# Performance work log

Hardware: AMD Instinct MI355X
Metric: run time of the kernel (lower is better)

The kernel has to match this reference:

```python
import jax, jax.numpy as jnp
import numpy as np

LEAKY_ALPHA = 0.2  # tf.nn.leaky_relu default

def setup_inputs() -> dict:
    key = jax.random.key(0)
    k1, k2, k3 = jax.random.split(key, 3)
    B, N, F, U = 4, 4096, 128, 64
    x = jax.random.normal(k1, (B, N, F), dtype=jnp.float32)
    W = jax.random.normal(k2, (F, U), dtype=jnp.float32) * (1.0 / np.sqrt(F))
    a = jax.random.normal(k3, (2 * U, 1), dtype=jnp.float32) * (1.0 / np.sqrt(2 * U))
    return {"x": x, "W": W, "a": a}

def reference(x, W, a):
    # h: (B, N, U)
    h = jnp.einsum('bnf,fu->bnu', x, W)
    U = h.shape[-1]
    a1 = a[:U, 0]   # attends to source node i
    a2 = a[U:, 0]   # attends to target node j
    # a^T [h_i || h_j] = a1^T h_i + a2^T h_j  (same math, no O(N^2*2U) concat)
    f1 = jnp.einsum('bnu,u->bn', h, a1)  # (B, N)
    f2 = jnp.einsum('bnu,u->bn', h, a2)  # (B, N)
    e = f1[:, :, None] + f2[:, None, :]  # (B, N, N)
    e = jnp.where(e >= 0, e, LEAKY_ALPHA * e)
    attn = jax.nn.softmax(e, axis=-1)    # softmax over j
    return jnp.einsum('bij,bju->biu', attn, h)
```

## Files before the change

kernel.cpp:

```cpp
#include <hip/hip_runtime.h>
#include <hip/hip_bf16.h>

#define NBATCH 4
#define NN 4096
#define NF 128
#define NU 64
#define CH 16
#define NCH (NN / CH)
#define LEAKY 0.2f

__global__ __launch_bounds__(256) void k1_h(
    const float* __restrict__ x, const float* __restrict__ W,
    const float* __restrict__ a,
    float* __restrict__ h, float* __restrict__ f1, float* __restrict__ f2) {
  __shared__ float xs[16][NF];
  int tid = threadIdx.x;
  int row0 = blockIdx.x * 16;
  const float4* xg = (const float4*)(x + (size_t)row0 * NF);
  float4* xs4 = (float4*)xs;
  for (int k = tid; k < 16 * NF / 4; k += 256) xs4[k] = xg[k];
  __syncthreads();
  int u = tid & 63;
  int wv = tid >> 6;
  float acc[4] = {0.f, 0.f, 0.f, 0.f};
#pragma unroll 4
  for (int f = 0; f < NF; f += 4) {
    float w0 = W[(f+0)*NU+u], w1 = W[(f+1)*NU+u],
          w2 = W[(f+2)*NU+u], w3 = W[(f+3)*NU+u];
#pragma unroll
    for (int r = 0; r < 4; ++r) {
      float4 xv = *(const float4*)&xs[wv*4+r][f];
      acc[r] += xv.x*w0 + xv.y*w1 + xv.z*w2 + xv.w*w3;
    }
  }
  float a1 = a[u], a2 = a[NU+u];
#pragma unroll
  for (int r = 0; r < 4; ++r) {
    int grow = row0 + wv*4 + r;
    h[(size_t)grow*NU+u] = acc[r];
    float p1 = acc[r]*a1, p2 = acc[r]*a2;
#pragma unroll
    for (int off = 32; off >= 1; off >>= 1) {
      p1 += __shfl_xor(p1, off, 64);
      p2 += __shfl_xor(p2, off, 64);
    }
    if (u == 0) { f1[grow] = p1; f2[grow] = p2; }
  }
}

__global__ __launch_bounds__(256) void k2a_count(
    const float* __restrict__ f2, unsigned short* __restrict__ pc) {
  __shared__ float fsk[256];
  int b = blockIdx.x >> 7;
  int jc = (blockIdx.x >> 4) & 7;
  int kc = blockIdx.x & 15;
  int tid = threadIdx.x;
  const float* f2b = f2 + b * NN;
  fsk[tid] = f2b[kc * 256 + tid];
  __syncthreads();
  int j0 = jc * 512 + tid;
  int j1 = j0 + 256;
  float my0 = f2b[j0], my1 = f2b[j1];
  int k0g = kc * 256;
  int cnt0 = 0, cnt1 = 0;
#pragma unroll 8
  for (int k = 0; k < 256; k += 4) {
    float4 v = *(const float4*)&fsk[k];
    int kg = k0g + k;
    cnt0 += (v.x < my0) || (v.x == my0 && kg + 0 < j0);
    cnt0 += (v.y < my0) || (v.y == my0 && kg + 1 < j0);
    cnt0 += (v.z < my0) || (v.z == my0 && kg + 2 < j0);
    cnt0 += (v.w < my0) || (v.w == my0 && kg + 3 < j0);
    cnt1 += (v.x < my1) || (v.x == my1 && kg + 0 < j1);
    cnt1 += (v.y < my1) || (v.y == my1 && kg + 1 < j1);
    cnt1 += (v.z < my1) || (v.z == my1 && kg + 2 < j1);
    cnt1 += (v.w < my1) || (v.w == my1 && kg + 3 < j1);
  }
  size_t base = ((size_t)(b * 16 + kc)) * NN;
  pc[base + j0] = (unsigned short)cnt0;
  pc[base + j1] = (unsigned short)cnt1;
}

__global__ __launch_bounds__(256) void k2b_scatter(
    const float* __restrict__ f2, const unsigned short* __restrict__ pc,
    float4* __restrict__ sdat, float* __restrict__ f2s) {
  int b = blockIdx.x >> 4;
  int jc = blockIdx.x & 15;
  int j = jc * 256 + threadIdx.x;
  float my = f2[b * NN + j];
  int rank = 0;
#pragma unroll
  for (int kc = 0; kc < 16; ++kc)
    rank += pc[((size_t)(b * 16 + kc)) * NN + j];
  int o = b * NN + rank;
  float4 v;
  v.x = my; v.y = expf(my); v.z = expf(LEAKY * my); v.w = __int_as_float(j);
  sdat[o] = v;
  f2s[o] = my;
}

__global__ __launch_bounds__(256) void k3_csum(
    const float* __restrict__ h, const float4* __restrict__ sdat,
    float* __restrict__ Pvhi, float* __restrict__ Pvlo,
    float* __restrict__ Pshi, float* __restrict__ Pslo) {
  int u = threadIdx.x & 63;
  int wv = threadIdx.x >> 6;
  int cg = blockIdx.x * 4 + wv;
  int b = cg >> 8;
  int c = cg & (NCH - 1);
  int k0 = b * NN + c * CH;
  const float* hb = h + (size_t)b * NN * NU;
  float ah = 0.f, al = 0.f, sh = 0.f, sl = 0.f;
#pragma unroll
  for (int k = 0; k < CH; ++k) {
    float4 e = sdat[k0 + k];
    int j = __float_as_int(e.w);
    float hv = hb[(size_t)j * NU + u];
    ah += e.y * hv; al += e.z * hv; sh += e.y; sl += e.z;
  }
  size_t o = (size_t)(b * (NCH + 1) + c) * NU + u;
  Pvhi[o] = ah; Pvlo[o] = al;
  if (u == 0) { Pshi[b * (NCH + 1) + c] = sh; Pslo[b * (NCH + 1) + c] = sl; }
}

__global__ __launch_bounds__(256) void k3b_scan(
    float* __restrict__ Pvhi, float* __restrict__ Pvlo,
    float* __restrict__ Pshi, float* __restrict__ Pslo) {
  int wid = blockIdx.x * 4 + (threadIdx.x >> 6);
  int l = threadIdx.x & 63;
  if (wid < 512) {
    int b = wid >> 7;
    int half = (wid >> 6) & 1;
    int u = wid & 63;
    float* T = half ? Pvlo : Pvhi;
    size_t i0 = (size_t)(b * (NCH + 1) + 4 * l) * NU + u;
    float v0 = T[i0], v1 = T[i0 + NU], v2 = T[i0 + 2*NU], v3 = T[i0 + 3*NU];
    float lsum = v0 + v1 + v2 + v3, s = lsum;
#pragma unroll
    for (int off = 1; off < 64; off <<= 1) {
      float t = __shfl_up(s, off, 64);
      if (l >= off) s += t;
    }
    float e = s - lsum;
    T[i0] = e;
    T[i0 + NU] = e + v0;
    T[i0 + 2*NU] = e + v0 + v1;
    T[i0 + 3*NU] = e + v0 + v1 + v2;
    if (l == 63) T[(size_t)(b * (NCH + 1) + NCH) * NU + u] = s;
  } else if (wid < 520) {
    int s2 = wid - 512;
    int b = s2 >> 1;
    float* T = (s2 & 1) ? Pslo : Pshi;
    int i0 = b * (NCH + 1) + 4 * l;
    float v0 = T[i0], v1 = T[i0 + 1], v2 = T[i0 + 2], v3 = T[i0 + 3];
    float lsum = v0 + v1 + v2 + v3, s = lsum;
#pragma unroll
    for (int off = 1; off < 64; off <<= 1) {
      float t = __shfl_up(s, off, 64);
      if (l >= off) s += t;
    }
    float e = s - lsum;
    T[i0] = e; T[i0 + 1] = e + v0; T[i0 + 2] = e + v0 + v1;
    T[i0 + 3] = e + v0 + v1 + v2;
    if (l == 63) T[b * (NCH + 1) + NCH] = s;
  }
}

__global__ __launch_bounds__(256) void k4_out(
    const float* __restrict__ f1, const float* __restrict__ f2s,
    const float* __restrict__ h, const float4* __restrict__ sdat,
    const float* __restrict__ Pvhi, const float* __restrict__ Pvlo,
    const float* __restrict__ Pshi, const float* __restrict__ Pslo,
    float* __restrict__ out) {
  int u = threadIdx.x & 63;
  int wv = threadIdx.x >> 6;
  int row = blockIdx.x * 4 + wv;
  int b = row >> 12;
  const float* fs = f2s + b * NN;
  float fv = f1[row];
  float theta = -fv;
  float q1 = fs[u * 64 + 63];
  int n1 = __popcll(__ballot(q1 < theta));
  int t;
  if (n1 == 64) {
    t = NN;
  } else {
    float q2 = fs[n1 * 64 + u];
    t = n1 * 64 + __popcll(__ballot(q2 < theta));
  }
  int c = t >> 4; if (c > NCH - 1) c = NCH - 1;
  int k0 = b * NN + c * CH;
  const float* hb = h + (size_t)b * NN * NU;
  float ch = 0.f, cl = 0.f, csh = 0.f, csl = 0.f;
#pragma unroll
  for (int k = 0; k < CH; ++k) {
    int kg = c * CH + k;
    float4 e = sdat[k0 + k];
    int j = __float_as_int(e.w);
    float hv = hb[(size_t)j * NU + u];
    bool hi = (kg >= t);
    float wH = hi ? e.y : 0.f;
    float wL = hi ? 0.f : e.z;
    ch += wH * hv; cl += wL * hv; csh += wH; csl += wL;
  }
  size_t base = (size_t)b * (NCH + 1);
  size_t oc0 = (base + c) * NU + u;
  size_t oc1 = (base + c + 1) * NU + u;
  size_t oT  = (base + NCH) * NU + u;
  float Ahi = (Pvhi[oT] - Pvhi[oc1]) + ch;
  float Alo = Pvlo[oc0] + cl;
  float Shi = (Pshi[base + NCH] - Pshi[base + c + 1]) + csh;
  float Slo = Pslo[base + c] + csl;
  float e1 = expf(fv), e1l = expf(LEAKY * fv);
  float den = e1 * Shi + e1l * Slo;
  out[(size_t)row * NU + u] = (e1 * Ahi + e1l * Alo) / den;
}

extern "C" void kernel_launch(void* const* d_in, const int* in_sizes, int n_in,
                              void* d_out, int out_size, void* d_ws, size_t ws_size,
                              hipStream_t stream) {
  const float* x = (const float*)d_in[0];
  const float* W = (const float*)d_in[1];
  const float* a = (const float*)d_in[2];
  float* out = (float*)d_out;
  float* ws = (float*)d_ws;

  size_t o = 0;
  float* h    = ws + o; o += (size_t)NBATCH * NN * NU;
  float* f1   = ws + o; o += (size_t)NBATCH * NN;
  float* f2   = ws + o; o += (size_t)NBATCH * NN;
  float* f2s  = ws + o; o += (size_t)NBATCH * NN;
  float4* sdat = (float4*)(ws + o); o += (size_t)NBATCH * NN * 4;
  float* Pvhi = ws + o; o += (size_t)NBATCH * (NCH + 1) * NU;
  float* Pvlo = ws + o; o += (size_t)NBATCH * (NCH + 1) * NU;
  float* Pshi = ws + o; o += (size_t)NBATCH * (NCH + 1);
  float* Pslo = ws + o; o += (size_t)NBATCH * (NCH + 1);
  unsigned short* pc = (unsigned short*)(ws + o); o += (size_t)NBATCH * 16 * NN / 2;

  k1_h<<<(NBATCH * NN) / 16, 256, 0, stream>>>(x, W, a, h, f1, f2);
  k2a_count<<<512, 256, 0, stream>>>(f2, pc);
  k2b_scatter<<<NBATCH * 16, 256, 0, stream>>>(f2, pc, sdat, f2s);
  k3_csum<<<(NBATCH * NCH) / 4, 256, 0, stream>>>(h, sdat, Pvhi, Pvlo, Pshi, Pslo);
  k3b_scan<<<130, 256, 0, stream>>>(Pvhi, Pvlo, Pshi, Pslo);
  k4_out<<<(NBATCH * NN) / 4, 256, 0, stream>>>(f1, f2s, h, sdat,
      Pvhi, Pvlo, Pshi, Pslo, out);
}
```

Before: 112.5 us.

## Fuse six GAT kernels into one cooperative persistent kernel with grid syncs

Replaces the six separate kernel launches (projection, rank count, scatter, chunk sums, scan, output) with one cooperative kernel of 512 blocks that separates the phases with grid.sync(). Per-block work is resized to fit 512 blocks, for example 32 rows per block in the projection and 8 output rows per wave. The aim is to remove launch and inter-kernel gap overhead, which matters at this small total time. In exchange the kernel depends on cooperative-launch residency and pays for five grid-wide barriers, and some phases leave most threads idle.

Result: slower. 406.4 us (+261.4%).

```diff
diff --git a/kernel.cpp b/kernel.cpp
--- a/kernel.cpp
+++ b/kernel.cpp
@@ -1,5 +1,8 @@
 #include <hip/hip_runtime.h>
+#include <hip/hip_cooperative_groups.h>
 #include <hip/hip_bf16.h>
+
+namespace cg = cooperative_groups;
 
 #define NBATCH 4
 #define NN 4096
@@ -8,212 +11,219 @@
 #define CH 16
 #define NCH (NN / CH)
 #define LEAKY 0.2f
-
-__global__ __launch_bounds__(256) void k1_h(
+#define NB 512
+
+__global__ __launch_bounds__(256, 2) void fused_gat(
     const float* __restrict__ x, const float* __restrict__ W,
-    const float* __restrict__ a,
-    float* __restrict__ h, float* __restrict__ f1, float* __restrict__ f2) {
-  __shared__ float xs[16][NF];
+    const float* __restrict__ a, float* __restrict__ h,
+    float* __restrict__ f1, float* __restrict__ f2,
+    unsigned short* __restrict__ pc, float4* __restrict__ sdat,
+    float* __restrict__ f2s, float* __restrict__ Pvhi,
+    float* __restrict__ Pvlo, float* __restrict__ Pshi,
+    float* __restrict__ Pslo, float* __restrict__ out) {
+  cg::grid_group grid = cg::this_grid();
+  __shared__ float smem[32 * NF];
   int tid = threadIdx.x;
-  int row0 = blockIdx.x * 16;
-  const float4* xg = (const float4*)(x + (size_t)row0 * NF);
-  float4* xs4 = (float4*)xs;
-  for (int k = tid; k < 16 * NF / 4; k += 256) xs4[k] = xg[k];
-  __syncthreads();
-  int u = tid & 63;
+  int blk = blockIdx.x;
+  int lane = tid & 63;
   int wv = tid >> 6;
-  float acc[4] = {0.f, 0.f, 0.f, 0.f};
+
+  {
+    float (*xs)[NF] = (float (*)[NF])smem;
+    int row0 = blk * 32;
+    const float4* xg = (const float4*)(x + (size_t)row0 * NF);
+    float4* xs4 = (float4*)smem;
+    for (int k = tid; k < 32 * NF / 4; k += 256) xs4[k] = xg[k];
+    __syncthreads();
+    int u = lane;
+    float acc[8] = {0.f,0.f,0.f,0.f,0.f,0.f,0.f,0.f};
 #pragma unroll 4
-  for (int f = 0; f < NF; f += 4) {
-    float w0 = W[(f+0)*NU+u], w1 = W[(f+1)*NU+u],
-          w2 = W[(f+2)*NU+u], w3 = W[(f+3)*NU+u];
-#pragma unroll
-    for (int r = 0; r < 4; ++r) {
-      float4 xv = *(const float4*)&xs[wv*4+r][f];
-      acc[r] += xv.x*w0 + xv.y*w1 + xv.z*w2 + xv.w*w3;
-    }
-  }
-  float a1 = a[u], a2 = a[NU+u];
-#pragma unroll
-  for (int r = 0; r < 4; ++r) {
-    int grow = row0 + wv*4 + r;
-    h[(size_t)grow*NU+u] = acc[r];
-    float p1 = acc[r]*a1, p2 = acc[r]*a2;
-#pragma unroll
-    for (int off = 32; off >= 1; off >>= 1) {
-      p1 += __shfl_xor(p1, off, 64);
-      p2 += __shfl_xor(p2, off, 64);
-    }
-    if (u == 0) { f1[grow] = p1; f2[grow] = p2; }
-  }
-}
-
-__global__ __launch_bounds__(256) void k2a_count(
-    const float* __restrict__ f2, unsigned short* __restrict__ pc) {
-  __shared__ float fsk[256];
-  int b = blockIdx.x >> 7;
-  int jc = (blockIdx.x >> 4) & 7;
-  int kc = blockIdx.x & 15;
-  int tid = threadIdx.x;
-  const float* f2b = f2 + b * NN;
-  fsk[tid] = f2b[kc * 256 + tid];
-  __syncthreads();
-  int j0 = jc * 512 + tid;
-  int j1 = j0 + 256;
-  float my0 = f2b[j0], my1 = f2b[j1];
-  int k0g = kc * 256;
-  int cnt0 = 0, cnt1 = 0;
+    for (int f = 0; f < NF; f += 4) {
+      float w0 = W[(f+0)*NU+u], w1 = W[(f+1)*NU+u],
+            w2 = W[(f+2)*NU+u], w3 = W[(f+3)*NU+u];
+#pragma unroll
+      for (int r = 0; r < 8; ++r) {
+        float4 xv = *(const float4*)&xs[wv*8+r][f];
+        acc[r] += xv.x*w0 + xv.y*w1 + xv.z*w2 + xv.w*w3;
+      }
+    }
+    float a1 = a[u], a2 = a[NU+u];
+#pragma unroll
+    for (int r = 0; r < 8; ++r) {
+      int grow = row0 + wv*8 + r;
+      h[(size_t)grow*NU+u] = acc[r];
+      float p1 = acc[r]*a1, p2 = acc[r]*a2;
+#pragma unroll
+      for (int off = 32; off >= 1; off >>= 1) {
+        p1 += __shfl_xor(p1, off, 64);
+        p2 += __shfl_xor(p2, off, 64);
+      }
+      if (u == 0) { f1[grow] = p1; f2[grow] = p2; }
+    }
+  }
+  grid.sync();
+
+  {
+    float* fsk = smem;
+    int b = blk >> 7;
+    int jc = (blk >> 4) & 7;
+    int kc = blk & 15;
+    const float* f2b = f2 + b * NN;
+    fsk[tid] = f2b[kc * 256 + tid];
+    __syncthreads();
+    int j0 = jc * 512 + tid;
+    int j1 = j0 + 256;
+    float my0 = f2b[j0], my1 = f2b[j1];
+    int k0g = kc * 256;
+    int cnt0 = 0, cnt1 = 0;
 #pragma unroll 8
-  for (int k = 0; k < 256; k += 4) {
-    float4 v = *(const float4*)&fsk[k];
-    int kg = k0g + k;
-    cnt0 += (v.x < my0) || (v.x == my0 && kg + 0 < j0);
-    cnt0 += (v.y < my0) || (v.y == my0 && kg + 1 < j0);
-    cnt0 += (v.z < my0) || (v.z == my0 && kg + 2 < j0);
-    cnt0 += (v.w < my0) || (v.w == my0 && kg + 3 < j0);
-    cnt1 += (v.x < my1) || (v.x == my1 && kg + 0 < j1);
-    cnt1 += (v.y < my1) || (v.y == my1 && kg + 1 < j1);
-    cnt1 += (v.z < my1) || (v.z == my1 && kg + 2 < j1);
-    cnt1 += (v.w < my1) || (v.w == my1 && kg + 3 < j1);
-  }
-  size_t base = ((size_t)(b * 16 + kc)) * NN;
-  pc[base + j0] = (unsigned short)cnt0;
-  pc[base + j1] = (unsigned short)cnt1;
-}
-
-__global__ __launch_bounds__(256) void k2b_scatter(
-    const float* __restrict__ f2, const unsigned short* __restrict__ pc,
-    float4* __restrict__ sdat, float* __restrict__ f2s) {
-  int b = blockIdx.x >> 4;
-  int jc = blockIdx.x & 15;
-  int j = jc * 256 + threadIdx.x;
-  float my = f2[b * NN + j];
-  int rank = 0;
-#pragma unroll
-  for (int kc = 0; kc < 16; ++kc)
-    rank += pc[((size_t)(b * 16 + kc)) * NN + j];
-  int o = b * NN + rank;
-  float4 v;
-  v.x = my; v.y = expf(my); v.z = expf(LEAKY * my); v.w = __int_as_float(j);
-  sdat[o] = v;
-  f2s[o] = my;
-}
-
-__global__ __launch_bounds__(256) void k3_csum(
-    const float* __restrict__ h, const float4* __restrict__ sdat,
-    float* __restrict__ Pvhi, float* __restrict__ Pvlo,
-    float* __restrict__ Pshi, float* __restrict__ Pslo) {
-  int u = threadIdx.x & 63;
-  int wv = threadIdx.x >> 6;
-  int cg = blockIdx.x * 4 + wv;
-  int b = cg >> 8;
-  int c = cg & (NCH - 1);
-  int k0 = b * NN + c * CH;
-  const float* hb = h + (size_t)b * NN * NU;
-  float ah = 0.f, al = 0.f, sh = 0.f, sl = 0.f;
-#pragma unroll
-  for (int k = 0; k < CH; ++k) {
-    float4 e = sdat[k0 + k];
-    int j = __float_as_int(e.w);
-    float hv = hb[(size_t)j * NU + u];
-    ah += e.y * hv; al += e.z * hv; sh += e.y; sl += e.z;
-  }
-  size_t o = (size_t)(b * (NCH + 1) + c) * NU + u;
-  Pvhi[o] = ah; Pvlo[o] = al;
-  if (u == 0) { Pshi[b * (NCH + 1) + c] = sh; Pslo[b * (NCH + 1) + c] = sl; }
-}
-
-__global__ __launch_bounds__(256) void k3b_scan(
-    float* __restrict__ Pvhi, float* __restrict__ Pvlo,
-    float* __restrict__ Pshi, float* __restrict__ Pslo) {
-  int wid = blockIdx.x * 4 + (threadIdx.x >> 6);
-  int l = threadIdx.x & 63;
-  if (wid < 512) {
-    int b = wid >> 7;
-    int half = (wid >> 6) & 1;
-    int u = wid & 63;
-    float* T = half ? Pvlo : Pvhi;
-    size_t i0 = (size_t)(b * (NCH + 1) + 4 * l) * NU + u;
-    float v0 = T[i0], v1 = T[i0 + NU], v2 = T[i0 + 2*NU], v3 = T[i0 + 3*NU];
-    float lsum = v0 + v1 + v2 + v3, s = lsum;
-#pragma unroll
-    for (int off = 1; off < 64; off <<= 1) {
-      float t = __shfl_up(s, off, 64);
-      if (l >= off) s += t;
-    }
-    float e = s - lsum;
-    T[i0] = e;
-    T[i0 + NU] = e + v0;
-    T[i0 + 2*NU] = e + v0 + v1;
-    T[i0 + 3*NU] = e + v0 + v1 + v2;
-    if (l == 63) T[(size_t)(b * (NCH + 1) + NCH) * NU + u] = s;
-  } else if (wid < 520) {
-    int s2 = wid - 512;
-    int b = s2 >> 1;
-    float* T = (s2 & 1) ? Pslo : Pshi;
-    int i0 = b * (NCH + 1) + 4 * l;
-    float v0 = T[i0], v1 = T[i0 + 1], v2 = T[i0 + 2], v3 = T[i0 + 3];
-    float lsum = v0 + v1 + v2 + v3, s = lsum;
-#pragma unroll
-    for (int off = 1; off < 64; off <<= 1) {
-      float t = __shfl_up(s, off, 64);
-      if (l >= off) s += t;
-    }
-    float e = s - lsum;
-    T[i0] = e; T[i0 + 1] = e + v0; T[i0 + 2] = e + v0 + v1;
-    T[i0 + 3] = e + v0 + v1 + v2;
-    if (l == 63) T[b * (NCH + 1) + NCH] = s;
-  }
-}
-
-__global__ __launch_bounds__(256) void k4_out(
-    const float* __restrict__ f1, const float* __restrict__ f2s,
-    const float* __restrict__ h, const float4* __restrict__ sdat,
-    const float* __restrict__ Pvhi, const float* __restrict__ Pvlo,
-    const float* __restrict__ Pshi, const float* __restrict__ Pslo,
-    float* __restrict__ out) {
-  int u = threadIdx.x & 63;
-  int wv = threadIdx.x >> 6;
-  int row = blockIdx.x * 4 + wv;
-  int b = row >> 12;
-  const float* fs = f2s + b * NN;
-  float fv = f1[row];
-  float theta = -fv;
-  float q1 = fs[u * 64 + 63];
-  int n1 = __popcll(__ballot(q1 < theta));
-  int t;
-  if (n1 == 64) {
-    t = NN;
-  } else {
-    float q2 = fs[n1 * 64 + u];
-    t = n1 * 64 + __popcll(__ballot(q2 < theta));
-  }
-  int c = t >> 4; if (c > NCH - 1) c = NCH - 1;
-  int k0 = b * NN + c * CH;
-  const float* hb = h + (size_t)b * NN * NU;
-  float ch = 0.f, cl = 0.f, csh = 0.f, csl = 0.f;
-#pragma unroll
-  for (int k = 0; k < CH; ++k) {
-    int kg = c * CH + k;
-    float4 e = sdat[k0 + k];
-    int j = __float_as_int(e.w);
-    float hv = hb[(size_t)j * NU + u];
-    bool hi = (kg >= t);
-    float wH = hi ? e.y : 0.f;
-    float wL = hi ? 0.f : e.z;
-    ch += wH * hv; cl += wL * hv; csh += wH; csl += wL;
-  }
-  size_t base = (size_t)b * (NCH + 1);
-  size_t oc0 = (base + c) * NU + u;
-  size_t oc1 = (base + c + 1) * NU + u;
-  size_t oT  = (base + NCH) * NU + u;
-  float Ahi = (Pvhi[oT] - Pvhi[oc1]) + ch;
-  float Alo = Pvlo[oc0] + cl;
-  float Shi = (Pshi[base + NCH] - Pshi[base + c + 1]) + csh;
-  float Slo = Pslo[base + c] + csl;
-  float e1 = expf(fv), e1l = expf(LEAKY * fv);
-  float den = e1 * Shi + e1l * Slo;
-  out[(size_t)row * NU + u] = (e1 * Ahi + e1l * Alo) / den;
+    for (int k = 0; k < 256; k += 4) {
+      float4 v = *(const float4*)&fsk[k];
+      int kg = k0g + k;
+      cnt0 += (v.x < my0) || (v.x == my0 && kg + 0 < j0);
+      cnt0 += (v.y < my0) || (v.y == my0 && kg + 1 < j0);
+      cnt0 += (v.z < my0) || (v.z == my0 && kg + 2 < j0);
+      cnt0 += (v.w < my0) || (v.w == my0 && kg + 3 < j0);
+      cnt1 += (v.x < my1) || (v.x == my1 && kg + 0 < j1);
+      cnt1 += (v.y < my1) || (v.y == my1 && kg + 1 < j1);
+      cnt1 += (v.z < my1) || (v.z == my1 && kg + 2 < j1);
+      cnt1 += (v.w < my1) || (v.w == my1 && kg + 3 < j1);
+    }
+    size_t base = ((size_t)(b * 16 + kc)) * NN;
+    pc[base + j0] = (unsigned short)cnt0;
+    pc[base + j1] = (unsigned short)cnt1;
+  }
+  grid.sync();
+
+  if (tid < 32) {
+    int g = blk * 32 + tid;
+    int b = g >> 12;
+    int j = g & (NN - 1);
+    float my = f2[b * NN + j];
+    int rank = 0;
+#pragma unroll
+    for (int kc = 0; kc < 16; ++kc)
+      rank += pc[((size_t)(b * 16 + kc)) * NN + j];
+    int o = b * NN + rank;
+    float4 v;
+    v.x = my; v.y = expf(my); v.z = expf(LEAKY * my); v.w = __int_as_float(j);
+    sdat[o] = v;
+    f2s[o] = my;
+  }
+  grid.sync();
+
+  {
+    int w = blk * 4 + wv;
+    if (w < NBATCH * NCH) {
+      int b = w >> 8;
+      int c = w & (NCH - 1);
+      int k0 = b * NN + c * CH;
+      const float* hb = h + (size_t)b * NN * NU;
+      int u = lane;
+      float ah = 0.f, al = 0.f, sh = 0.f, sl = 0.f;
+#pragma unroll
+      for (int k = 0; k < CH; ++k) {
+        float4 e = sdat[k0 + k];
+        int j = __float_as_int(e.w);
+        float hv = hb[(size_t)j * NU + u];
+        ah += e.y * hv; al += e.z * hv; sh += e.y; sl += e.z;
+      }
+      size_t o = (size_t)(b * (NCH + 1) + c) * NU + u;
+      Pvhi[o] = ah; Pvlo[o] = al;
+      if (u == 0) { Pshi[b * (NCH + 1) + c] = sh; Pslo[b * (NCH + 1) + c] = sl; }
+    }
+  }
+  grid.sync();
+
+  {
+    int wid = blk * 4 + wv;
+    int l = lane;
+    if (wid < 512) {
+      int b = wid >> 7;
+      int half = (wid >> 6) & 1;
+      int u = wid & 63;
+      float* T = half ? Pvlo : Pvhi;
+      size_t i0 = (size_t)(b * (NCH + 1) + 4 * l) * NU + u;
+      float v0 = T[i0], v1 = T[i0 + NU], v2 = T[i0 + 2*NU], v3 = T[i0 + 3*NU];
+      float lsum = v0 + v1 + v2 + v3, s = lsum;
+#pragma unroll
+      for (int off = 1; off < 64; off <<= 1) {
+        float t = __shfl_up(s, off, 64);
+        if (l >= off) s += t;
+      }
+      float e = s - lsum;
+      T[i0] = e;
+      T[i0 + NU] = e + v0;
+      T[i0 + 2*NU] = e + v0 + v1;
+      T[i0 + 3*NU] = e + v0 + v1 + v2;
+      if (l == 63) T[(size_t)(b * (NCH + 1) + NCH) * NU + u] = s;
+    } else if (wid < 520) {
+      int s2 = wid - 512;
+      int b = s2 >> 1;
+      float* T = (s2 & 1) ? Pslo : Pshi;
+      int i0 = b * (NCH + 1) + 4 * l;
+      float v0 = T[i0], v1 = T[i0 + 1], v2 = T[i0 + 2], v3 = T[i0 + 3];
+      float lsum = v0 + v1 + v2 + v3, s = lsum;
+#pragma unroll
+      for (int off = 1; off < 64; off <<= 1) {
+        float t = __shfl_up(s, off, 64);
+        if (l >= off) s += t;
+      }
+      float e = s - lsum;
+      T[i0] = e; T[i0 + 1] = e + v0; T[i0 + 2] = e + v0 + v1;
+      T[i0 + 3] = e + v0 + v1 + v2;
+      if (l == 63) T[b * (NCH + 1) + NCH] = s;
+    }
+  }
+  grid.sync();
+
+  {
+    int u = lane;
+    int wbase = (blk * 4 + wv) * 8;
+#pragma unroll 2
+    for (int rr = 0; rr < 8; ++rr) {
+      int row = wbase + rr;
+      int b = row >> 12;
+      const float* fs = f2s + b * NN;
+      float fv = f1[row];
+      float theta = -fv;
+      float q1 = fs[u * 64 + 63];
+      int n1 = __popcll(__ballot(q1 < theta));
+      int t;
+      if (n1 == 64) {
+        t = NN;
+      } else {
+        float q2 = fs[n1 * 64 + u];
+        t = n1 * 64 + __popcll(__ballot(q2 < theta));
+      }
+      int c = t >> 4; if (c > NCH - 1) c = NCH - 1;
+      int k0 = b * NN + c * CH;
+      const float* hb = h + (size_t)b * NN * NU;
+      float ch = 0.f, cl = 0.f, csh = 0.f, csl = 0.f;
+#pragma unroll
+      for (int k = 0; k < CH; ++k) {
+        int kg = c * CH + k;
+        float4 e = sdat[k0 + k];
+        int j = __float_as_int(e.w);
+        float hv = hb[(size_t)j * NU + u];
+        bool hi = (kg >= t);
+        float wH = hi ? e.y : 0.f;
+        float wL = hi ? 0.f : e.z;
+        ch += wH * hv; cl += wL * hv; csh += wH; csl += wL;
+      }
+      size_t base = (size_t)b * (NCH + 1);
+      size_t oc0 = (base + c) * NU + u;
+      size_t oc1 = (base + c + 1) * NU + u;
+      size_t oT  = (base + NCH) * NU + u;
+      float Ahi = (Pvhi[oT] - Pvhi[oc1]) + ch;
+      float Alo = Pvlo[oc0] + cl;
+      float Shi = (Pshi[base + NCH] - Pshi[base + c + 1]) + csh;
+      float Slo = Pslo[base + c] + csl;
+      float e1 = expf(fv), e1l = expf(LEAKY * fv);
+      float den = e1 * Shi + e1l * Slo;
+      out[(size_t)row * NU + u] = (e1 * Ahi + e1l * Alo) / den;
+    }
+  }
 }
 
 extern "C" void kernel_launch(void* const* d_in, const int* in_sizes, int n_in,
@@ -237,11 +247,11 @@
   float* Pslo = ws + o; o += (size_t)NBATCH * (NCH + 1);
   unsigned short* pc = (unsigned short*)(ws + o); o += (size_t)NBATCH * 16 * NN / 2;
 
-  k1_h<<<(NBATCH * NN) / 16, 256, 0, stream>>>(x, W, a, h, f1, f2);
-  k2a_count<<<512, 256, 0, stream>>>(f2, pc);
-  k2b_scatter<<<NBATCH * 16, 256, 0, stream>>>(f2, pc, sdat, f2s);
-  k3_csum<<<(NBATCH * NCH) / 4, 256, 0, stream>>>(h, sdat, Pvhi, Pvlo, Pshi, Pslo);
-  k3b_scan<<<130, 256, 0, stream>>>(Pvhi, Pvlo, Pshi, Pslo);
-  k4_out<<<(NBATCH * NN) / 4, 256, 0, stream>>>(f1, f2s, h, sdat,
-      Pvhi, Pvlo, Pshi, Pslo, out);
+  void* kargs[] = {
+    (void*)&x, (void*)&W, (void*)&a, (void*)&h, (void*)&f1, (void*)&f2,
+    (void*)&pc, (void*)&sdat, (void*)&f2s,
+    (void*)&Pvhi, (void*)&Pvlo, (void*)&Pshi, (void*)&Pslo, (void*)&out
+  };
+  hipLaunchCooperativeKernel((const void*)fused_gat, dim3(NB), dim3(256),
+                             kargs, 0, stream);
 }
```
